# Performance work log

Hardware: AMD Instinct MI355X
Metric: run time of the kernel (lower is better)

Reference implementation:

```python
import jax, jax.numpy as jnp
import numpy as np


def setup_inputs() -> dict:
    key = jax.random.key(0)
    k1, k2, k3, k4 = jax.random.split(key, 4)
    N, K, F, E = 50000, 32, 128, 16
    nodes = jax.random.normal(k1, (N, F), dtype=jnp.float32)
    nlist = jax.random.randint(k2, (N, K), 0, N, dtype=jnp.int64)
    edges = jax.random.uniform(k3, (N, K, E), dtype=jnp.float32)
    w = jax.random.normal(k4, (F, F, E), dtype=jnp.float32) * 0.05
    return {"nodes": nodes, "nlist": nlist, "edges": edges, "w": w}


def reference(nodes, nlist, edges, w):
    # gather neighbor features: [N, K, F]
    sliced = nodes[nlist]
    K = nlist.shape[1]
    # fused 3-way contraction + mean over neighbors (axis j):
    # original: einsum('ijn,ijl,lmn->ijm', edges, sliced, w).mean(axis=1)
    out = jnp.einsum('ijn,ijl,lmn->im', edges, sliced, w) / K
    return out
```

## Files before the change

### kernel.cpp

```cpp
#include <hip/hip_runtime.h>


typedef _Float16 half8  __attribute__((ext_vector_type(8)));
typedef _Float16 half4v __attribute__((ext_vector_type(4)));
typedef float    float4v __attribute__((ext_vector_type(4)));
typedef int      int4v  __attribute__((ext_vector_type(4)));
typedef unsigned int uint;

#define NF 128
#define NK 32
#define NE 16
#define RPB 32

__global__ __launch_bounds__(256) void k_prep_nodes(const float* __restrict__ src,
                                                    _Float16* __restrict__ dst, int n4) {
    int i = blockIdx.x * 256 + threadIdx.x;
    if (i < n4) {
        float4v v = ((const float4v*)src)[i];
        half4v h;
        h[0] = (_Float16)v[0]; h[1] = (_Float16)v[1];
        h[2] = (_Float16)v[2]; h[3] = (_Float16)v[3];
        ((half4v*)dst)[i] = h;
    }
}

__global__ __launch_bounds__(256) void k_prep_w(const float* __restrict__ w,
                                                _Float16* __restrict__ w2t) {
    int o  = blockIdx.x * 256 + threadIdx.x;
    int m  = o >> 11;
    int cf = o & 2047;
    int ch = cf >> 9;
    int cp = cf & 511;
    int ltq = cp >> 6;
    int n   = (cp >> 2) & 15;
    int g   = cp & 3;
    int l = ch * 32 + (ltq >> 2) * 16 + (ltq & 3) * 4 + g;
    w2t[o] = (_Float16)w[(l * NF + m) * NE + n];
}

__global__ __launch_bounds__(256, 4) void k_mp(const _Float16* __restrict__ nodes_h,
                                               const int* __restrict__ nlist,
                                               const float* __restrict__ edges,
                                               const _Float16* __restrict__ w2t,
                                               float* __restrict__ out, int N) {
    __shared__ __align__(16) _Float16 s_T[RPB * 512];
    __shared__ __align__(16) _Float16 s_G[4 * NK * 32];

    const int tid  = threadIdx.x;
    const int wv   = tid >> 6;
    const int ln   = tid & 63;
    const int quad = ln >> 4;
    const int c16  = ln & 15;
    const int row0 = blockIdx.x * RPB;

    _Float16* __restrict__ gbuf = &s_G[wv * (NK * 32)];
    const float4v zf = {0.f, 0.f, 0.f, 0.f};

    half8 fe[8];
    #pragma unroll
    for (int r = 0; r < 8; ++r) {
        int rg = row0 + wv * 8 + r; if (rg > N - 1) rg = N - 1;
        const float* ep = edges + (size_t)rg * (NK * NE) + quad * (8 * NE) + c16;
        #pragma unroll
        for (int jj = 0; jj < 8; ++jj) fe[r][jj] = (_Float16)ep[jj * NE];
    }

    const int jlane = ln >> 2;
    const int sub   = ln & 3;
    int nb0[8], nb1[8];
    #pragma unroll
    for (int r = 0; r < 8; ++r) {
        int rg = row0 + wv * 8 + r; if (rg > N - 1) rg = N - 1;
        nb0[r] = nlist[rg * NK + jlane]      << 8;
        nb1[r] = nlist[rg * NK + 16 + jlane] << 8;
    }
    const int wblk0 = (sub ^ ((jlane >> 3) & 3)) << 3;
    const int wblk1 = (sub ^ (((jlane + 16) >> 3) & 3)) << 3;

    float4v a00 = zf, a01 = zf, a10 = zf, a11 = zf;
    const char* nbase = (const char*)nodes_h;

    for (int ch = 0; ch < 4; ++ch) {
        #pragma unroll
        for (int r = 0; r < 8; ++r) {
            const int il = wv * 8 + r;
            half8 g0 = *(const half8*)(nbase + nb0[r] + ch * 64 + sub * 16);
            half8 g1 = *(const half8*)(nbase + nb1[r] + ch * 64 + sub * 16);
            *(half8*)&gbuf[jlane * 32 + wblk0]        = g0;
            *(half8*)&gbuf[(jlane + 16) * 32 + wblk1] = g1;
            #pragma unroll
            for (int lt = 0; lt < 2; ++lt) {
                const int col   = lt * 16 + c16;
                const int rbase = quad * (8 * 32) + (col ^ (quad << 3));
                uint t0 = *(const unsigned short*)&gbuf[rbase + 0 * 32];
                uint t1 = *(const unsigned short*)&gbuf[rbase + 1 * 32];
                uint t2 = *(const unsigned short*)&gbuf[rbase + 2 * 32];
                uint t3 = *(const unsigned short*)&gbuf[rbase + 3 * 32];
                uint t4 = *(const unsigned short*)&gbuf[rbase + 4 * 32];
                uint t5 = *(const unsigned short*)&gbuf[rbase + 5 * 32];
                uint t6 = *(const unsigned short*)&gbuf[rbase + 6 * 32];
                uint t7 = *(const unsigned short*)&gbuf[rbase + 7 * 32];
                int4v pv;
                pv[0] = (int)(t0 | (t1 << 16));
                pv[1] = (int)(t2 | (t3 << 16));
                pv[2] = (int)(t4 | (t5 << 16));
                pv[3] = (int)(t6 | (t7 << 16));
                half8 av = __builtin_bit_cast(half8, pv);
                float4v d = __builtin_amdgcn_mfma_f32_16x16x32_f16(av, fe[r], zf, 0, 0, 0);
                const int ltq  = lt * 4 + quad;
                const int cb   = ltq * 64 + c16 * 4;
                const int phys = cb ^ ((((ltq ^ il) & 7)) << 3);
                half4v hv;
                hv[0] = (_Float16)d[0]; hv[1] = (_Float16)d[1];
                hv[2] = (_Float16)d[2]; hv[3] = (_Float16)d[3];
                *(half4v*)&s_T[il * 512 + phys] = hv;
            }
        }
        __syncthreads();

        const _Float16* wr0 = w2t + ((size_t)(wv * 2 + 0) * 16 + c16) * 2048 + ch * 512;
        const _Float16* wr1 = w2t + ((size_t)(wv * 2 + 1) * 16 + c16) * 2048 + ch * 512;
        #pragma unroll 4
        for (int kt = 0; kt < 16; ++kt) {
            const int cb2  = kt * 32 + quad * 8;
            const int mask = (((cb2 >> 6) ^ c16) & 7) << 3;
            half8 t0 = *(const half8*)&s_T[c16 * 512        + (cb2 ^ mask)];
            half8 t1 = *(const half8*)&s_T[(16 + c16) * 512 + (cb2 ^ mask)];
            half8 b0 = *(const half8*)(wr0 + cb2);
            half8 b1 = *(const half8*)(wr1 + cb2);
            a00 = __builtin_amdgcn_mfma_f32_16x16x32_f16(t0, b0, a00, 0, 0, 0);
            a10 = __builtin_amdgcn_mfma_f32_16x16x32_f16(t1, b0, a10, 0, 0, 0);
            a01 = __builtin_amdgcn_mfma_f32_16x16x32_f16(t0, b1, a01, 0, 0, 0);
            a11 = __builtin_amdgcn_mfma_f32_16x16x32_f16(t1, b1, a11, 0, 0, 0);
        }
        __syncthreads();
    }

    const float sc = 1.0f / (float)NK;
    const int mb = (wv << 5) + c16;
    #pragma unroll
    for (int g = 0; g < 4; ++g) {
        int i0 = row0 + quad * 4 + g;
        int i1 = i0 + 16;
        if (i0 < N) {
            out[(size_t)i0 * NF + mb]      = a00[g] * sc;
            out[(size_t)i0 * NF + mb + 16] = a01[g] * sc;
        }
        if (i1 < N) {
            out[(size_t)i1 * NF + mb]      = a10[g] * sc;
            out[(size_t)i1 * NF + mb + 16] = a11[g] * sc;
        }
    }
}

extern "C" void kernel_launch(void* const* d_in, const int* in_sizes, int n_in,
                              void* d_out, int out_size, void* d_ws, size_t ws_size,
                              hipStream_t stream) {
    const float* nodes = (const float*)d_in[0];
    const int*   nlist = (const int*)d_in[1];
    const float* edges = (const float*)d_in[2];
    const float* w     = (const float*)d_in[3];
    float* out = (float*)d_out;

    const int N = in_sizes[0] / NF;

    _Float16* w2t     = (_Float16*)d_ws;
    _Float16* nodes_h = (_Float16*)((char*)d_ws + 524288);

    const int n4 = (N * NF) / 4;
    k_prep_nodes<<<(n4 + 255) / 256, 256, 0, stream>>>(nodes, nodes_h, n4);
    k_prep_w<<<(NF * NF * NE) / 256, 256, 0, stream>>>(w, w2t);

    const int blocks = (N + RPB - 1) / RPB;
    k_mp<<<blocks, 256, 0, stream>>>(nodes_h, nlist, edges, w2t, out, N);
}
```

Before: 336.9 us.

## Stream neighbor gathers directly into LDS with async prefetch and smaller feature chunks

```diff
diff --git a/kernel.cpp b/kernel.cpp
--- a/kernel.cpp
+++ b/kernel.cpp
@@ -11,6 +11,11 @@
 #define NK 32
 #define NE 16
 #define RPB 32
+
+__device__ __forceinline__ void load_lds4(const void* g, void* l) {
+    __builtin_amdgcn_global_load_lds((const __attribute__((address_space(1))) void*)g,
+                                     (__attribute__((address_space(3))) void*)l, 4, 0, 0);
+}
 
 __global__ __launch_bounds__(256) void k_prep_nodes(const float* __restrict__ src,
                                                     _Float16* __restrict__ dst, int n4) {
@@ -29,22 +34,23 @@
     int o  = blockIdx.x * 256 + threadIdx.x;
     int m  = o >> 11;
     int cf = o & 2047;
-    int ch = cf >> 9;
-    int cp = cf & 511;
-    int ltq = cp >> 6;
-    int n   = (cp >> 2) & 15;
-    int g   = cp & 3;
-    int l = ch * 32 + (ltq >> 2) * 16 + (ltq & 3) * 4 + g;
+    int ch = cf >> 8;
+    int cp = cf & 255;
+    int q  = cp >> 6;
+    int n  = (cp >> 2) & 15;
+    int g  = cp & 3;
+    int l  = ch * 16 + q * 4 + g;
     w2t[o] = (_Float16)w[(l * NF + m) * NE + n];
 }
 
-__global__ __launch_bounds__(256, 4) void k_mp(const _Float16* __restrict__ nodes_h,
+__global__ __launch_bounds__(256, 5) void k_mp(const _Float16* __restrict__ nodes_h,
                                                const int* __restrict__ nlist,
                                                const float* __restrict__ edges,
                                                const _Float16* __restrict__ w2t,
                                                float* __restrict__ out, int N) {
-    __shared__ __align__(16) _Float16 s_T[RPB * 512];
-    __shared__ __align__(16) _Float16 s_G[4 * NK * 32];
+    __shared__ __align__(16) _Float16 s_T[RPB * 256];
+    __shared__ __align__(16) uint s_Ga[4 * 272];
+    __shared__ __align__(16) uint s_Gb[4 * 272];
 
     const int tid  = threadIdx.x;
     const int wv   = tid >> 6;
@@ -53,7 +59,8 @@
     const int c16  = ln & 15;
     const int row0 = blockIdx.x * RPB;
 
-    _Float16* __restrict__ gbuf = &s_G[wv * (NK * 32)];
+    uint* __restrict__ gAw = &s_Ga[wv * 272];
+    uint* __restrict__ gBw = &s_Gb[wv * 272];
     const float4v zf = {0.f, 0.f, 0.f, 0.f};
 
     half8 fe[8];
@@ -65,67 +72,66 @@
         for (int jj = 0; jj < 8; ++jj) fe[r][jj] = (_Float16)ep[jj * NE];
     }
 
-    const int jlane = ln >> 2;
-    const int sub   = ln & 3;
-    int nb0[8], nb1[8];
+    int nbj[8];
     #pragma unroll
     for (int r = 0; r < 8; ++r) {
         int rg = row0 + wv * 8 + r; if (rg > N - 1) rg = N - 1;
-        nb0[r] = nlist[rg * NK + jlane]      << 8;
-        nb1[r] = nlist[rg * NK + 16 + jlane] << 8;
+        nbj[r] = nlist[rg * NK + (ln & 31)] << 8;
     }
-    const int wblk0 = (sub ^ ((jlane >> 3) & 3)) << 3;
-    const int wblk1 = (sub ^ (((jlane + 16) >> 3) & 3)) << 3;
+    const char* gsrc = (const char*)nodes_h + ((ln >> 5) << 2);
 
     float4v a00 = zf, a01 = zf, a10 = zf, a11 = zf;
-    const char* nbase = (const char*)nodes_h;
+    const uint psel = 0x05040100u + (uint)(c16 & 1) * 0x02020202u;
 
-    for (int ch = 0; ch < 4; ++ch) {
+    {
+        const char* sp0 = gsrc + nbj[0];
+        const char* sp1 = gsrc + nbj[1];
+        #pragma unroll
+        for (int p = 0; p < 4; ++p) load_lds4(sp0 + p * 8, gAw + p * 68);
+        #pragma unroll
+        for (int p = 0; p < 4; ++p) load_lds4(sp1 + p * 8, gBw + p * 68);
+    }
+
+    for (int ch = 0; ch < 8; ++ch) {
         #pragma unroll
         for (int r = 0; r < 8; ++r) {
             const int il = wv * 8 + r;
-            half8 g0 = *(const half8*)(nbase + nb0[r] + ch * 64 + sub * 16);
-            half8 g1 = *(const half8*)(nbase + nb1[r] + ch * 64 + sub * 16);
-            *(half8*)&gbuf[jlane * 32 + wblk0]        = g0;
-            *(half8*)&gbuf[(jlane + 16) * 32 + wblk1] = g1;
-            #pragma unroll
-            for (int lt = 0; lt < 2; ++lt) {
-                const int col   = lt * 16 + c16;
-                const int rbase = quad * (8 * 32) + (col ^ (quad << 3));
-                uint t0 = *(const unsigned short*)&gbuf[rbase + 0 * 32];
-                uint t1 = *(const unsigned short*)&gbuf[rbase + 1 * 32];
-                uint t2 = *(const unsigned short*)&gbuf[rbase + 2 * 32];
-                uint t3 = *(const unsigned short*)&gbuf[rbase + 3 * 32];
-                uint t4 = *(const unsigned short*)&gbuf[rbase + 4 * 32];
-                uint t5 = *(const unsigned short*)&gbuf[rbase + 5 * 32];
-                uint t6 = *(const unsigned short*)&gbuf[rbase + 6 * 32];
-                uint t7 = *(const unsigned short*)&gbuf[rbase + 7 * 32];
-                int4v pv;
-                pv[0] = (int)(t0 | (t1 << 16));
-                pv[1] = (int)(t2 | (t3 << 16));
-                pv[2] = (int)(t4 | (t5 << 16));
-                pv[3] = (int)(t6 | (t7 << 16));
-                half8 av = __builtin_bit_cast(half8, pv);
-                float4v d = __builtin_amdgcn_mfma_f32_16x16x32_f16(av, fe[r], zf, 0, 0, 0);
-                const int ltq  = lt * 4 + quad;
-                const int cb   = ltq * 64 + c16 * 4;
-                const int phys = cb ^ ((((ltq ^ il) & 7)) << 3);
-                half4v hv;
-                hv[0] = (_Float16)d[0]; hv[1] = (_Float16)d[1];
-                hv[2] = (_Float16)d[2]; hv[3] = (_Float16)d[3];
-                *(half4v*)&s_T[il * 512 + phys] = hv;
+            uint* cw = (r & 1) ? gBw : gAw;
+            __builtin_amdgcn_s_waitcnt(0x0F74);
+            const int ro = (c16 >> 2) * 68 + ((c16 >> 1) & 1) * 32 + quad * 8;
+            uint4 lo = *(const uint4*)(cw + ro);
+            uint4 hi = *(const uint4*)(cw + ro + 4);
+            uint a0v = __builtin_amdgcn_perm(lo.y, lo.x, psel);
+            uint a1v = __builtin_amdgcn_perm(lo.w, lo.z, psel);
+            uint a2v = __builtin_amdgcn_perm(hi.y, hi.x, psel);
+            uint a3v = __builtin_amdgcn_perm(hi.w, hi.z, psel);
+            int4v pv; pv[0] = (int)a0v; pv[1] = (int)a1v; pv[2] = (int)a2v; pv[3] = (int)a3v;
+            half8 av = __builtin_bit_cast(half8, pv);
+            if (ch * 8 + r < 62) {
+                const int r2  = (r + 2) & 7;
+                const int ch2 = ch + ((r + 2) >> 3);
+                const char* sp = gsrc + nbj[r2] + ch2 * 32;
+                #pragma unroll
+                for (int p = 0; p < 4; ++p) load_lds4(sp + p * 8, cw + p * 68);
             }
+            float4v d = __builtin_amdgcn_mfma_f32_16x16x32_f16(av, fe[r], zf, 0, 0, 0);
+            const int cb   = (quad << 6) + (c16 << 2);
+            const int phys = cb ^ ((((cb >> 6) ^ il) & 7) << 3);
+            half4v hv;
+            hv[0] = (_Float16)d[0]; hv[1] = (_Float16)d[1];
+            hv[2] = (_Float16)d[2]; hv[3] = (_Float16)d[3];
+            *(half4v*)&s_T[il * 256 + phys] = hv;
         }
         __syncthreads();
 
-        const _Float16* wr0 = w2t + ((size_t)(wv * 2 + 0) * 16 + c16) * 2048 + ch * 512;
-        const _Float16* wr1 = w2t + ((size_t)(wv * 2 + 1) * 16 + c16) * 2048 + ch * 512;
-        #pragma unroll 4
-        for (int kt = 0; kt < 16; ++kt) {
-            const int cb2  = kt * 32 + quad * 8;
+        const _Float16* wr0 = w2t + ((size_t)((wv * 2 + 0) * 16 + c16)) * 2048 + ch * 256;
+        const _Float16* wr1 = w2t + ((size_t)((wv * 2 + 1) * 16 + c16)) * 2048 + ch * 256;
+        #pragma unroll
+        for (int kt = 0; kt < 8; ++kt) {
+            const int cb2  = (kt << 5) + (quad << 3);
             const int mask = (((cb2 >> 6) ^ c16) & 7) << 3;
-            half8 t0 = *(const half8*)&s_T[c16 * 512        + (cb2 ^ mask)];
-            half8 t1 = *(const half8*)&s_T[(16 + c16) * 512 + (cb2 ^ mask)];
+            half8 t0 = *(const half8*)&s_T[c16 * 256        + (cb2 ^ mask)];
+            half8 t1 = *(const half8*)&s_T[(16 + c16) * 256 + (cb2 ^ mask)];
             half8 b0 = *(const half8*)(wr0 + cb2);
             half8 b1 = *(const half8*)(wr1 + cb2);
             a00 = __builtin_amdgcn_mfma_f32_16x16x32_f16(t0, b0, a00, 0, 0, 0);
@@ -140,7 +146,7 @@
     const int mb = (wv << 5) + c16;
     #pragma unroll
     for (int g = 0; g < 4; ++g) {
-        int i0 = row0 + quad * 4 + g;
+        int i0 = row0 + (quad << 2) + g;
         int i1 = i0 + 16;
         if (i0 < N) {
             out[(size_t)i0 * NF + mb]      = a00[g] * sc;
```

Result: slower. 513.3 us (+52.3%).

## Warp-specialize message-passing kernel into producer and consumer waves with double-buffered LDS

Applied to the files above, without the earlier changes.

```diff
diff --git a/kernel.cpp b/kernel.cpp
--- a/kernel.cpp
+++ b/kernel.cpp
@@ -10,41 +10,42 @@
 #define NF 128
 #define NK 32
 #define NE 16
-#define RPB 32
+#define RPB 16
 
-__global__ __launch_bounds__(256) void k_prep_nodes(const float* __restrict__ src,
-                                                    _Float16* __restrict__ dst, int n4) {
-    int i = blockIdx.x * 256 + threadIdx.x;
-    if (i < n4) {
-        float4v v = ((const float4v*)src)[i];
-        half4v h;
-        h[0] = (_Float16)v[0]; h[1] = (_Float16)v[1];
-        h[2] = (_Float16)v[2]; h[3] = (_Float16)v[3];
-        ((half4v*)dst)[i] = h;
+__global__ __launch_bounds__(256) void k_prep(const float* __restrict__ nodes,
+                                              const float* __restrict__ w,
+                                              _Float16* __restrict__ nodes_h,
+                                              _Float16* __restrict__ w2t, int n4) {
+    const int b = blockIdx.x;
+    if (b < 1024) {
+        int o  = b * 256 + threadIdx.x;
+        int m  = o >> 11;
+        int cf = o & 2047;
+        int ch = cf >> 9;
+        int cp = cf & 511;
+        int ltq = cp >> 6;
+        int n   = (cp >> 2) & 15;
+        int g   = cp & 3;
+        int l = ch * 32 + (ltq >> 2) * 16 + (ltq & 3) * 4 + g;
+        w2t[o] = (_Float16)w[(l * NF + m) * NE + n];
+    } else {
+        int i = (b - 1024) * 256 + threadIdx.x;
+        if (i < n4) {
+            float4v v = ((const float4v*)nodes)[i];
+            half4v h;
+            h[0] = (_Float16)v[0]; h[1] = (_Float16)v[1];
+            h[2] = (_Float16)v[2]; h[3] = (_Float16)v[3];
+            ((half4v*)nodes_h)[i] = h;
+        }
     }
 }
 
-__global__ __launch_bounds__(256) void k_prep_w(const float* __restrict__ w,
-                                                _Float16* __restrict__ w2t) {
-    int o  = blockIdx.x * 256 + threadIdx.x;
-    int m  = o >> 11;
-    int cf = o & 2047;
-    int ch = cf >> 9;
-    int cp = cf & 511;
-    int ltq = cp >> 6;
-    int n   = (cp >> 2) & 15;
-    int g   = cp & 3;
-    int l = ch * 32 + (ltq >> 2) * 16 + (ltq & 3) * 4 + g;
-    w2t[o] = (_Float16)w[(l * NF + m) * NE + n];
-}
-
-__global__ __launch_bounds__(256, 4) void k_mp(const _Float16* __restrict__ nodes_h,
+__global__ __launch_bounds__(768, 6) void k_mp(const _Float16* __restrict__ nodes_h,
                                                const int* __restrict__ nlist,
                                                const float* __restrict__ edges,
                                                const _Float16* __restrict__ w2t,
                                                float* __restrict__ out, int N) {
-    __shared__ __align__(16) _Float16 s_T[RPB * 512];
-    __shared__ __align__(16) _Float16 s_G[4 * NK * 32];
+    __shared__ __align__(16) _Float16 s_T[2][RPB * 512];
 
     const int tid  = threadIdx.x;
     const int wv   = tid >> 6;
@@ -52,103 +53,102 @@
     const int quad = ln >> 4;
     const int c16  = ln & 15;
     const int row0 = blockIdx.x * RPB;
-
-    _Float16* __restrict__ gbuf = &s_G[wv * (NK * 32)];
     const float4v zf = {0.f, 0.f, 0.f, 0.f};
 
-    half8 fe[8];
-    #pragma unroll
-    for (int r = 0; r < 8; ++r) {
-        int rg = row0 + wv * 8 + r; if (rg > N - 1) rg = N - 1;
-        const float* ep = edges + (size_t)rg * (NK * NE) + quad * (8 * NE) + c16;
+    if (wv < 8) {
+        const int p = wv;
+        half8 fe[2];
+        int vb[2][8];
         #pragma unroll
-        for (int jj = 0; jj < 8; ++jj) fe[r][jj] = (_Float16)ep[jj * NE];
-    }
+        for (int r = 0; r < 2; ++r) {
+            const int rg = row0 + p * 2 + r;
+            const float* ep = edges + (size_t)rg * (NK * NE) + quad * (8 * NE) + c16;
+            #pragma unroll
+            for (int jj = 0; jj < 8; ++jj) fe[r][jj] = (_Float16)ep[jj * NE];
+            #pragma unroll
+            for (int jj = 0; jj < 8; ++jj)
+                vb[r][jj] = nlist[rg * NK + quad * 8 + jj] << 8;
+        }
+        const char* gb = (const char*)nodes_h + ((c16 >> 1) << 2);
+        const uint psel = 0x05040100u + (uint)(c16 & 1) * 0x02020202u;
 
-    const int jlane = ln >> 2;
-    const int sub   = ln & 3;
-    int nb0[8], nb1[8];
-    #pragma unroll
-    for (int r = 0; r < 8; ++r) {
-        int rg = row0 + wv * 8 + r; if (rg > N - 1) rg = N - 1;
-        nb0[r] = nlist[rg * NK + jlane]      << 8;
-        nb1[r] = nlist[rg * NK + 16 + jlane] << 8;
-    }
-    const int wblk0 = (sub ^ ((jlane >> 3) & 3)) << 3;
-    const int wblk1 = (sub ^ (((jlane + 16) >> 3) & 3)) << 3;
+        uint dwA[16], dwB[16];
+        #pragma unroll
+        for (int q = 0; q < 16; ++q)
+            dwA[q] = *(const uint*)(gb + vb[0][q & 7] + ((q >> 3) << 5));
 
-    float4v a00 = zf, a01 = zf, a10 = zf, a11 = zf;
-    const char* nbase = (const char*)nodes_h;
+        #pragma unroll
+        for (int ch = 0; ch < 4; ++ch) {
+            #pragma unroll
+            for (int r = 0; r < 2; ++r) {
+                const int t = ch * 2 + r;
+                uint* cur = (t & 1) ? dwB : dwA;
+                uint* nxt = (t & 1) ? dwA : dwB;
+                if (t < 7) {
+                    const int t1 = t + 1, ch1 = t1 >> 1, r1 = t1 & 1;
+                    #pragma unroll
+                    for (int q = 0; q < 16; ++q)
+                        nxt[q] = *(const uint*)(gb + vb[r1][q & 7] + (ch1 << 6) + ((q >> 3) << 5));
+                }
+                __builtin_amdgcn_sched_barrier(0);
+                const int il = p * 2 + r;
+                #pragma unroll
+                for (int lt = 0; lt < 2; ++lt) {
+                    int4v pv;
+                    pv[0] = (int)__builtin_amdgcn_perm(cur[lt*8+1], cur[lt*8+0], psel);
+                    pv[1] = (int)__builtin_amdgcn_perm(cur[lt*8+3], cur[lt*8+2], psel);
+                    pv[2] = (int)__builtin_amdgcn_perm(cur[lt*8+5], cur[lt*8+4], psel);
+                    pv[3] = (int)__builtin_amdgcn_perm(cur[lt*8+7], cur[lt*8+6], psel);
+                    half8 av = __builtin_bit_cast(half8, pv);
+                    float4v d = __builtin_amdgcn_mfma_f32_16x16x32_f16(av, fe[r], zf, 0, 0, 0);
+                    const int ltq  = lt * 4 + quad;
+                    const int cb   = ltq * 64 + c16 * 4;
+                    const int phys = cb ^ ((((ltq ^ il) & 7)) << 3);
+                    half4v hv;
+                    hv[0] = (_Float16)d[0]; hv[1] = (_Float16)d[1];
+                    hv[2] = (_Float16)d[2]; hv[3] = (_Float16)d[3];
+                    *(half4v*)&s_T[ch & 1][il * 512 + phys] = hv;
+                }
+            }
+            __syncthreads();
+        }
+    } else {
+        const int cw = wv - 8;
+        float4v a00 = zf, a01 = zf;
+        const _Float16* wr0 = w2t + ((size_t)((cw * 2 + 0) * 16 + c16)) * 2048;
+        const _Float16* wr1 = w2t + ((size_t)((cw * 2 + 1) * 16 + c16)) * 2048;
 
-    for (int ch = 0; ch < 4; ++ch) {
+#define CONSUME_CHUNK(cc)                                                          \
+        {                                                                          \
+            const _Float16* w0 = wr0 + (cc) * 512;                                 \
+            const _Float16* w1 = wr1 + (cc) * 512;                                 \
+            _Pragma("unroll")                                                      \
+            for (int kt = 0; kt < 16; ++kt) {                                      \
+                const int cb2  = kt * 32 + quad * 8;                               \
+                const int mask = (((cb2 >> 6) ^ c16) & 7) << 3;                    \
+                half8 t0 = *(const half8*)&s_T[(cc) & 1][c16 * 512 + (cb2 ^ mask)];\
+                half8 b0 = *(const half8*)(w0 + cb2);                              \
+                half8 b1 = *(const half8*)(w1 + cb2);                              \
+                a00 = __builtin_amdgcn_mfma_f32_16x16x32_f16(t0, b0, a00, 0, 0, 0);\
+                a01 = __builtin_amdgcn_mfma_f32_16x16x32_f16(t0, b1, a01, 0, 0, 0);\
+            }                                                                      \
+        }
+
         #pragma unroll
-        for (int r = 0; r < 8; ++r) {
-            const int il = wv * 8 + r;
-            half8 g0 = *(const half8*)(nbase + nb0[r] + ch * 64 + sub * 16);
-            half8 g1 = *(const half8*)(nbase + nb1[r] + ch * 64 + sub * 16);
-            *(half8*)&gbuf[jlane * 32 + wblk0]        = g0;
-            *(half8*)&gbuf[(jlane + 16) * 32 + wblk1] = g1;
-            #pragma unroll
-            for (int lt = 0; lt < 2; ++lt) {
-                const int col   = lt * 16 + c16;
-                const int rbase = quad * (8 * 32) + (col ^ (quad << 3));
-                uint t0 = *(const unsigned short*)&gbuf[rbase + 0 * 32];
-                uint t1 = *(const unsigned short*)&gbuf[rbase + 1 * 32];
-                uint t2 = *(const unsigned short*)&gbuf[rbase + 2 * 32];
-                uint t3 = *(const unsigned short*)&gbuf[rbase + 3 * 32];
-                uint t4 = *(const unsigned short*)&gbuf[rbase + 4 * 32];
-                uint t5 = *(const unsigned short*)&gbuf[rbase + 5 * 32];
-                uint t6 = *(const unsigned short*)&gbuf[rbase + 6 * 32];
-                uint t7 = *(const unsigned short*)&gbuf[rbase + 7 * 32];
-                int4v pv;
-                pv[0] = (int)(t0 | (t1 << 16));
-                pv[1] = (int)(t2 | (t3 << 16));
-                pv[2] = (int)(t4 | (t5 << 16));
-                pv[3] = (int)(t6 | (t7 << 16));
-                half8 av = __builtin_bit_cast(half8, pv);
-                float4v d = __builtin_amdgcn_mfma_f32_16x16x32_f16(av, fe[r], zf, 0, 0, 0);
-                const int ltq  = lt * 4 + quad;
-                const int cb   = ltq * 64 + c16 * 4;
-                const int phys = cb ^ ((((ltq ^ il) & 7)) << 3);
-                half4v hv;
-                hv[0] = (_Float16)d[0]; hv[1] = (_Float16)d[1];
-                hv[2] = (_Float16)d[2]; hv[3] = (_Float16)d[3];
-                *(half4v*)&s_T[il * 512 + phys] = hv;
-            }
+        for (int ch = 0; ch < 4; ++ch) {
+            if (ch > 0) CONSUME_CHUNK(ch - 1);
+            __syncthreads();
         }
-        __syncthreads();
+        CONSUME_CHUNK(3);
+#undef CONSUME_CHUNK
 
-        const _Float16* wr0 = w2t + ((size_t)(wv * 2 + 0) * 16 + c16) * 2048 + ch * 512;
-        const _Float16* wr1 = w2t + ((size_t)(wv * 2 + 1) * 16 + c16) * 2048 + ch * 512;
-        #pragma unroll 4
-        for (int kt = 0; kt < 16; ++kt) {
-            const int cb2  = kt * 32 + quad * 8;
-            const int mask = (((cb2 >> 6) ^ c16) & 7) << 3;
-            half8 t0 = *(const half8*)&s_T[c16 * 512        + (cb2 ^ mask)];
-            half8 t1 = *(const half8*)&s_T[(16 + c16) * 512 + (cb2 ^ mask)];
-            half8 b0 = *(const half8*)(wr0 + cb2);
-            half8 b1 = *(const half8*)(wr1 + cb2);
-            a00 = __builtin_amdgcn_mfma_f32_16x16x32_f16(t0, b0, a00, 0, 0, 0);
-            a10 = __builtin_amdgcn_mfma_f32_16x16x32_f16(t1, b0, a10, 0, 0, 0);
-            a01 = __builtin_amdgcn_mfma_f32_16x16x32_f16(t0, b1, a01, 0, 0, 0);
-            a11 = __builtin_amdgcn_mfma_f32_16x16x32_f16(t1, b1, a11, 0, 0, 0);
-        }
-        __syncthreads();
-    }
-
-    const float sc = 1.0f / (float)NK;
-    const int mb = (wv << 5) + c16;
-    #pragma unroll
-    for (int g = 0; g < 4; ++g) {
-        int i0 = row0 + quad * 4 + g;
-        int i1 = i0 + 16;
-        if (i0 < N) {
+        const float sc = 1.0f / (float)NK;
+        const int mb = cw * 32 + c16;
+        #pragma unroll
+        for (int g = 0; g < 4; ++g) {
+            const int i0 = row0 + quad * 4 + g;
             out[(size_t)i0 * NF + mb]      = a00[g] * sc;
             out[(size_t)i0 * NF + mb + 16] = a01[g] * sc;
-        }
-        if (i1 < N) {
-            out[(size_t)i1 * NF + mb]      = a10[g] * sc;
-            out[(size_t)i1 * NF + mb + 16] = a11[g] * sc;
         }
     }
 }
@@ -168,9 +168,9 @@
     _Float16* nodes_h = (_Float16*)((char*)d_ws + 524288);
 
     const int n4 = (N * NF) / 4;
-    k_prep_nodes<<<(n4 + 255) / 256, 256, 0, stream>>>(nodes, nodes_h, n4);
-    k_prep_w<<<(NF * NF * NE) / 256, 256, 0, stream>>>(w, w2t);
+    const int prep_blocks = 1024 + (n4 + 255) / 256;
+    k_prep<<<prep_blocks, 256, 0, stream>>>(nodes, w, nodes_h, w2t, n4);
 
-    const int blocks = (N + RPB - 1) / RPB;
-    k_mp<<<blocks, 256, 0, stream>>>(nodes_h, nlist, edges, w2t, out, N);
+    const int blocks = N / RPB;
+    k_mp<<<blocks, 768, 0, stream>>>(nodes_h, nlist, edges, w2t, out, N);
 }
```

New measurement: 431.6 us. 28.1% more time.
